# Optimization experiments

Hardware: AMD Instinct MI355X
Metric: run time of the kernel (lower is better)

## Reference

```python
import jax, jax.numpy as jnp
import numpy as np

D_MODEL = 1024
NUM_HEADS = 16
D_K = D_MODEL // NUM_HEADS


def setup_inputs() -> dict:
    key = jax.random.key(0)
    ks = jax.random.split(key, 9)
    s = 1.0 / np.sqrt(D_MODEL)
    x = jax.random.normal(ks[0], (4, 2048, D_MODEL), dtype=jnp.float32)
    Wq = jax.random.uniform(ks[1], (D_MODEL, D_MODEL), jnp.float32, -s, s)
    bq = jax.random.uniform(ks[2], (D_MODEL,), jnp.float32, -s, s)
    Wk = jax.random.uniform(ks[3], (D_MODEL, D_MODEL), jnp.float32, -s, s)
    bk = jax.random.uniform(ks[4], (D_MODEL,), jnp.float32, -s, s)
    Wv = jax.random.uniform(ks[5], (D_MODEL, D_MODEL), jnp.float32, -s, s)
    bv = jax.random.uniform(ks[6], (D_MODEL,), jnp.float32, -s, s)
    Wo = jax.random.uniform(ks[7], (D_MODEL, D_MODEL), jnp.float32, -s, s)
    bo = jax.random.uniform(ks[8], (D_MODEL,), jnp.float32, -s, s)
    return {"x": x, "Wq": Wq, "bq": bq, "Wk": Wk, "bk": bk,
            "Wv": Wv, "bv": bv, "Wo": Wo, "bo": bo}


def reference(x, Wq, bq, Wk, bk, Wv, bv, Wo, bo):
    B, S, _ = x.shape
    # Linear projections (torch Linear: x @ W.T + b)
    q = x @ Wq.T + bq
    k = x @ Wk.T + bk
    v = x @ Wv.T + bv
    # [B, H, S, d_k]
    q = q.reshape(B, S, NUM_HEADS, D_K).transpose(0, 2, 1, 3)
    k = k.reshape(B, S, NUM_HEADS, D_K).transpose(0, 2, 1, 3)
    v = v.reshape(B, S, NUM_HEADS, D_K).transpose(0, 2, 1, 3)
    score = jnp.einsum('bhqd,bhkd->bhqk', q, k) / jnp.sqrt(jnp.float32(D_K))
    causal = jnp.tril(jnp.ones((S, S), dtype=bool))  # True = keep
    score = jnp.where(causal[None, None], score, -jnp.inf)
    attn = jax.nn.softmax(score, axis=-1)
    out = jnp.einsum('bhqk,bhkd->bhqd', attn, v)
    out = out.transpose(0, 2, 1, 3).reshape(B, S, D_MODEL)
    return out @ Wo.T + bo
```

## Files before the change

### kernel.cpp

```cpp
#include <hip/hip_runtime.h>
#include <hip/hip_bf16.h>
#include <stdint.h>

#define D_MODEL 1024
#define SEQ     2048
#define BATCH   4
#define NHEAD   16
#define DKH     64
#define MTOT    (BATCH * SEQ)

typedef __bf16 bf16x8 __attribute__((ext_vector_type(8)));
typedef __bf16 bf16x4 __attribute__((ext_vector_type(4)));
typedef float  floatx4 __attribute__((ext_vector_type(4)));
typedef short  s16x4  __attribute__((ext_vector_type(4)));

#define GLOAD_LDS16(gp, lp)                                            \
    __builtin_amdgcn_global_load_lds(                                  \
        (const __attribute__((address_space(1))) unsigned int*)(gp),   \
        (__attribute__((address_space(3))) unsigned int*)(lp), 16, 0, 0)

#define MFMA16(a, b, c) __builtin_amdgcn_mfma_f32_16x16x32_bf16(a, b, c, 0, 0, 0)

#if __has_builtin(__builtin_amdgcn_exp2f)
#define EXP2(x) __builtin_amdgcn_exp2f(x)
#else
#define EXP2(x) exp2f(x)
#endif

static __device__ __forceinline__ floatx4 pv_mfma(s16x4 a, s16x4 b, floatx4 c)
{
#if __has_builtin(__builtin_amdgcn_mfma_f32_16x16x16bf16_1k)
    return __builtin_amdgcn_mfma_f32_16x16x16bf16_1k(a, b, c, 0, 0, 0);
#else
    asm("v_mfma_f32_16x16x16_bf16 %0, %1, %2, %0" : "+v"(c) : "v"(a), "v"(b));
    return c;
#endif
}

__global__ __launch_bounds__(256)
void cvt_x_kernel(const float* __restrict__ src, __bf16* __restrict__ dst)
{
    const int i = (blockIdx.x * 256 + threadIdx.x) * 4;
    floatx4 v = *(const floatx4*)(src + i);
    bf16x4 o;
    o[0] = (__bf16)v[0]; o[1] = (__bf16)v[1]; o[2] = (__bf16)v[2]; o[3] = (__bf16)v[3];
    *(bf16x4*)(dst + i) = o;
}

__global__ __launch_bounds__(256)
void cvt_w3_kernel(const float* __restrict__ Wq, const float* __restrict__ Wk,
                   const float* __restrict__ Wv, __bf16* __restrict__ Wcat)
{
    const int z = blockIdx.y;
    const float* src = (z == 0) ? Wq : ((z == 1) ? Wk : Wv);
    const int i = (blockIdx.x * 256 + threadIdx.x) * 4;
    floatx4 v = *(const floatx4*)(src + i);
    bf16x4 o;
    o[0] = (__bf16)v[0]; o[1] = (__bf16)v[1]; o[2] = (__bf16)v[2]; o[3] = (__bf16)v[3];
    *(bf16x4*)(Wcat + (size_t)z * (D_MODEL * D_MODEL) + i) = o;
}

__global__ __launch_bounds__(256)
void qkv_gemm_kernel(const __bf16* __restrict__ xb, const __bf16* __restrict__ Wcat,
                     const float* __restrict__ bq, const float* __restrict__ bk,
                     const float* __restrict__ bv,
                     __bf16* __restrict__ Q, __bf16* __restrict__ K,
                     __bf16* __restrict__ Vt)
{
    __shared__ __align__(16) char smem_raw[128 * 136 * 2];
    __bf16* As = (__bf16*)smem_raw;
    __bf16* Bs = (__bf16*)(smem_raw + 16384);
    __bf16* Cs = (__bf16*)smem_raw;

    const int t    = threadIdx.x;
    const int w    = t >> 6, l = t & 63, quad = l >> 4, r16 = l & 15;
    const int wm   = w & 1, wn = w >> 1;
    const int m0   = blockIdx.y * 128;
    const int n0   = blockIdx.x * 128;
    const int z    = n0 >> 10;
    const float* bias = (z == 0) ? bq : ((z == 1) ? bk : bv);
    __bf16* outQK     = (z == 0) ? Q  : K;
    const float scale = (z == 0) ? 0.18033688011112042f : 1.0f;

    floatx4 acc[4][4];
#pragma unroll
    for (int i = 0; i < 4; ++i)
#pragma unroll
        for (int j = 0; j < 4; ++j) acc[i][j] = (floatx4){0.f, 0.f, 0.f, 0.f};

    unsigned int* lAs = (unsigned int*)As;
    unsigned int* lBs = (unsigned int*)Bs;

    const int r0 = t >> 3;
    const int s0 = ((t & 7) ^ (r0 & 7)) * 8;
    const __bf16* Agp[4];
    const __bf16* Bgp[4];
#pragma unroll
    for (int i = 0; i < 4; ++i) {
        const int row = r0 + i * 32;
        const int sch8 = ((t & 7) ^ (row & 7)) * 8;
        Agp[i] = xb   + (size_t)(m0 + row) * 1024 + sch8;
        Bgp[i] = Wcat + (size_t)(n0 + row) * 1024 + sch8;
    }
    (void)s0;

    const int fsw0 = ((0 * 4 + quad) ^ (r16 & 7)) * 8;
    const int fsw1 = ((1 * 4 + quad) ^ (r16 & 7)) * 8;

    for (int k0 = 0; k0 < 1024; k0 += 64) {
        __syncthreads();
#pragma unroll
        for (int i = 0; i < 4; ++i) {
            const int c = t + 256 * i;
            GLOAD_LDS16(Agp[i] + k0, lAs + c * 4);
            GLOAD_LDS16(Bgp[i] + k0, lBs + c * 4);
        }
        __syncthreads();

#pragma unroll
        for (int kk = 0; kk < 2; ++kk) {
            const int fsw = (kk == 0) ? fsw0 : fsw1;
            bf16x8 af[4], bfm[4];
#pragma unroll
            for (int i = 0; i < 4; ++i)
                af[i] = *(const bf16x8*)&As[(wm * 64 + i * 16 + r16) * 64 + fsw];
#pragma unroll
            for (int j = 0; j < 4; ++j)
                bfm[j] = *(const bf16x8*)&Bs[(wn * 64 + j * 16 + r16) * 64 + fsw];
#pragma unroll
            for (int i = 0; i < 4; ++i)
#pragma unroll
                for (int j = 0; j < 4; ++j)
                    acc[i][j] = MFMA16(af[i], bfm[j], acc[i][j]);
        }
    }

    __syncthreads();

    if (z == 2) {
#pragma unroll
        for (int i = 0; i < 4; ++i) {
            const int mb = wm * 64 + i * 16 + quad * 4;
#pragma unroll
            for (int j = 0; j < 4; ++j) {
                const int nl = wn * 64 + j * 16 + r16;
                const float bb = bias[(n0 + nl) & 1023];
                bf16x4 p4;
#pragma unroll
                for (int r = 0; r < 4; ++r) p4[r] = (__bf16)(acc[i][j][r] + bb);
                *(bf16x4*)&Cs[nl * 136 + mb] = p4;
            }
        }
    } else {
#pragma unroll
        for (int i = 0; i < 4; ++i) {
            const int mb = wm * 64 + i * 16 + quad * 4;
#pragma unroll
            for (int j = 0; j < 4; ++j) {
                const int nl = wn * 64 + j * 16 + r16;
                const float bb = bias[(n0 + nl) & 1023];
#pragma unroll
                for (int r = 0; r < 4; ++r)
                    Cs[(mb + r) * 136 + nl] =
                        (__bf16)((acc[i][j][r] + bb) * scale);
            }
        }
    }
    __syncthreads();

    const int b  = m0 >> 11;
    if (z == 2) {
#pragma unroll
        for (int k = 0; k < 8; ++k) {
            const int nl = (t >> 4) + k * 16;
            const int ml = (t & 15) * 8;
            bf16x8 row = *(const bf16x8*)&Cs[nl * 136 + ml];
            const int f = (n0 + nl) & 1023, h = f >> 6, d = f & 63;
            const int s = (m0 & 2047) + ml;
            *(bf16x8*)&Vt[((size_t)((b * 16 + h) * 64 + d) << 11) + s] = row;
        }
    } else {
#pragma unroll
        for (int k = 0; k < 8; ++k) {
            const int ml = (t >> 4) + k * 16;
            const int nl = (t & 15) * 8;
            bf16x8 row = *(const bf16x8*)&Cs[ml * 136 + nl];
            const int f = (n0 + nl) & 1023, h = f >> 6, d = f & 63;
            const int s = (m0 & 2047) + ml;
            *(bf16x8*)&outQK[((size_t)(b * 16 + h) << 17) + ((size_t)s << 6) + d]
                = row;
        }
    }
}

__global__ __launch_bounds__(256)
void out_gemm_kernel(const __bf16* __restrict__ A, const __bf16* __restrict__ Wob,
                     const float* __restrict__ bo, float* __restrict__ out)
{
    __shared__ __align__(16) __bf16 As[128 * 64];
    __shared__ __align__(16) __bf16 Bs[128 * 64];

    const int t    = threadIdx.x;
    const int w    = t >> 6, l = t & 63, quad = l >> 4, r16 = l & 15;
    const int wm   = w & 1, wn = w >> 1;
    const int m0   = blockIdx.y * 128;
    const int n0   = blockIdx.x * 128;

    floatx4 acc[4][4];
#pragma unroll
    for (int i = 0; i < 4; ++i)
#pragma unroll
        for (int j = 0; j < 4; ++j) acc[i][j] = (floatx4){0.f, 0.f, 0.f, 0.f};

    unsigned int* lAs = (unsigned int*)As;
    unsigned int* lBs = (unsigned int*)Bs;

    const int r0 = t >> 3;
    const __bf16* Agp[4];
    const __bf16* Bgp[4];
#pragma unroll
    for (int i = 0; i < 4; ++i) {
        const int row = r0 + i * 32;
        const int sch8 = ((t & 7) ^ (row & 7)) * 8;
        Agp[i] = A   + (size_t)(m0 + row) * 1024 + sch8;
        Bgp[i] = Wob + (size_t)(n0 + row) * 1024 + sch8;
    }
    const int fsw0 = ((0 * 4 + quad) ^ (r16 & 7)) * 8;
    const int fsw1 = ((1 * 4 + quad) ^ (r16 & 7)) * 8;

    for (int k0 = 0; k0 < 1024; k0 += 64) {
        __syncthreads();
#pragma unroll
        for (int i = 0; i < 4; ++i) {
            const int c = t + 256 * i;
            GLOAD_LDS16(Agp[i] + k0, lAs + c * 4);
            GLOAD_LDS16(Bgp[i] + k0, lBs + c * 4);
        }
        __syncthreads();

#pragma unroll
        for (int kk = 0; kk < 2; ++kk) {
            const int fsw = (kk == 0) ? fsw0 : fsw1;
            bf16x8 af[4], bfm[4];
#pragma unroll
            for (int i = 0; i < 4; ++i)
                af[i] = *(const bf16x8*)&As[(wm * 64 + i * 16 + r16) * 64 + fsw];
#pragma unroll
            for (int j = 0; j < 4; ++j)
                bfm[j] = *(const bf16x8*)&Bs[(wn * 64 + j * 16 + r16) * 64 + fsw];
#pragma unroll
            for (int i = 0; i < 4; ++i)
#pragma unroll
                for (int j = 0; j < 4; ++j)
                    acc[i][j] = MFMA16(af[i], bfm[j], acc[i][j]);
        }
    }

#pragma unroll
    for (int i = 0; i < 4; ++i) {
        const int mg = m0 + wm * 64 + i * 16 + quad * 4;
#pragma unroll
        for (int j = 0; j < 4; ++j) {
            const int ng = n0 + wn * 64 + j * 16 + r16;
            const float bb = bo[ng];
#pragma unroll
            for (int r = 0; r < 4; ++r)
                out[(size_t)(mg + r) * 1024 + ng] = acc[i][j][r] + bb;
        }
    }
}

__global__ __launch_bounds__(256, 4)
void attn_kernel(const __bf16* __restrict__ Qg, const __bf16* __restrict__ Kg,
                 const __bf16* __restrict__ Vtg, __bf16* __restrict__ O)
{
    __shared__ __align__(16) __bf16 Ks[2][64 * 72];
    __shared__ __align__(16) __bf16 Vs[2][64 * 72];

    const int t    = threadIdx.x;
    const int w    = t >> 6, l = t & 63, quad = l >> 4, r16 = l & 15;
    const int bh   = blockIdx.x;
    const int y    = blockIdx.y;
    const int p    = y >> 1, half = y & 1;
    const int qa   = 15 - p, qb = p;
    const size_t base = (size_t)bh * SEQ * DKH;
    const int d0   = 2 * qa + half;
    const int d1   = 2 * qb + half;
    const int nkt  = d0 + 1;
    const int row0 = qa * 128 + half * 64 + w * 16;
    const int row1 = qb * 128 + half * 64 + w * 16;

    const s16x4 ones16 = {(short)0x3F80, (short)0x3F80,
                          (short)0x3F80, (short)0x3F80};

    bf16x8 qf00, qf01, qf10, qf11;
    qf00 = *(const bf16x8*)&Qg[base + (size_t)(row0 + r16) * 64 + quad * 8];
    qf01 = *(const bf16x8*)&Qg[base + (size_t)(row0 + r16) * 64 + 32 + quad * 8];
    qf10 = *(const bf16x8*)&Qg[base + (size_t)(row1 + r16) * 64 + quad * 8];
    qf11 = *(const bf16x8*)&Qg[base + (size_t)(row1 + r16) * 64 + 32 + quad * 8];

    floatx4 o[2][4];
#pragma unroll
    for (int mi = 0; mi < 2; ++mi)
#pragma unroll
        for (int j = 0; j < 4; ++j) o[mi][j] = (floatx4){0.f, 0.f, 0.f, 0.f};
    floatx4 osum[2];
    osum[0] = (floatx4){0.f, 0.f, 0.f, 0.f};
    osum[1] = (floatx4){0.f, 0.f, 0.f, 0.f};

    const int srow = t >> 3;
    const int sg   = (t & 7) * 8;

    bf16x8 kc0, kc1, vc0, vc1;
    kc0 = *(const bf16x8*)&Kg[base + (size_t)srow * 64 + sg];
    kc1 = *(const bf16x8*)&Kg[base + (size_t)(32 + srow) * 64 + sg];
    vc0 = *(const bf16x8*)&Vtg[base + (size_t)srow * 2048 + sg];
    vc1 = *(const bf16x8*)&Vtg[base + (size_t)(32 + srow) * 2048 + sg];

    for (int kt = 0; kt < nkt; ++kt) {
        __bf16* ks = Ks[kt & 1];
        __bf16* vs = Vs[kt & 1];
        *(bf16x8*)&ks[srow * 72 + sg] = kc0;
        *(bf16x8*)&ks[(32 + srow) * 72 + sg] = kc1;
        *(bf16x8*)&vs[srow * 72 + sg] = vc0;
        *(bf16x8*)&vs[(32 + srow) * 72 + sg] = vc1;
        if (kt + 1 < nkt) {
            const int kr = (kt + 1) * 64;
            kc0 = *(const bf16x8*)&Kg[base + (size_t)(kr + srow) * 64 + sg];
            kc1 = *(const bf16x8*)&Kg[base + (size_t)(kr + 32 + srow) * 64 + sg];
            vc0 = *(const bf16x8*)&Vtg[base + (size_t)srow * 2048 + kr + sg];
            vc1 = *(const bf16x8*)&Vtg[base + (size_t)(32 + srow) * 2048 + kr + sg];
        }
        __syncthreads();

        const bool a1 = (kt <= d1);
        __builtin_amdgcn_s_setprio(1);
        bf16x8 kf0, kf1;
#pragma unroll
        for (int j = 0; j < 4; ++j) {
            kf0 = *(const bf16x8*)&ks[(j * 16 + r16) * 72 + quad * 8];
            kf1 = *(const bf16x8*)&ks[(j * 16 + r16) * 72 + 32 + quad * 8];
            floatx4 z0 = (floatx4){0.f, 0.f, 0.f, 0.f};
            floatx4 z1 = (floatx4){0.f, 0.f, 0.f, 0.f};
            z0 = MFMA16(kf0, qf00, z0);
            z0 = MFMA16(kf1, qf01, z0);
            if (a1) {
                z1 = MFMA16(kf0, qf10, z1);
                z1 = MFMA16(kf1, qf11, z1);
            }
            const int kg = kt * 64 + j * 16 + quad * 4;
            bf16x4 pb0, pb1;
            if (kt < d0) {
#pragma unroll
                for (int r = 0; r < 4; ++r)
                    pb0[r] = (__bf16)EXP2(z0[r]);
            } else {
                const int qg0 = row0 + r16;
#pragma unroll
                for (int r = 0; r < 4; ++r) {
                    float pp = 0.f;
                    if (kg + r <= qg0) pp = EXP2(z0[r]);
                    pb0[r] = (__bf16)pp;
                }
            }
            s16x4 pa0 = __builtin_bit_cast(s16x4, pb0);
            s16x4 pa1;
            if (a1) {
                if (kt < d1) {
#pragma unroll
                    for (int r = 0; r < 4; ++r)
                        pb1[r] = (__bf16)EXP2(z1[r]);
                } else {
                    const int qg1 = row1 + r16;
#pragma unroll
                    for (int r = 0; r < 4; ++r) {
                        float pp = 0.f;
                        if (kg + r <= qg1) pp = EXP2(z1[r]);
                        pb1[r] = (__bf16)pp;
                    }
                }
                pa1 = __builtin_bit_cast(s16x4, pb1);
            }
            osum[0] = pv_mfma(pa0, ones16, osum[0]);
            if (a1) osum[1] = pv_mfma(pa1, ones16, osum[1]);
#pragma unroll
            for (int jd = 0; jd < 4; ++jd) {
                const s16x4 vv =
                    *(const s16x4*)&vs[(jd * 16 + r16) * 72 + j * 16 + quad * 4];
                o[0][jd] = pv_mfma(pa0, vv, o[0][jd]);
                if (a1) o[1][jd] = pv_mfma(pa1, vv, o[1][jd]);
            }
        }
        __builtin_amdgcn_s_setprio(0);
    }

    const int b = bh >> 4, h = bh & 15;
#pragma unroll
    for (int mi = 0; mi < 2; ++mi) {
        const int rowb = (mi == 0) ? row0 : row1;
#pragma unroll
        for (int r = 0; r < 4; ++r) {
            const int qrow = rowb + quad * 4 + r;
            const float inv = 1.f / osum[mi][r];
#pragma unroll
            for (int jd = 0; jd < 4; ++jd) {
                const int d = jd * 16 + r16;
                O[((size_t)(b * SEQ + qrow) * D_MODEL) + h * 64 + d] =
                    (__bf16)(o[mi][jd][r] * inv);
            }
        }
    }
}

extern "C" void kernel_launch(void* const* d_in, const int* in_sizes, int n_in,
                              void* d_out, int out_size, void* d_ws, size_t ws_size,
                              hipStream_t stream)
{
    (void)in_sizes; (void)n_in; (void)out_size; (void)ws_size;
    const float* x  = (const float*)d_in[0];
    const float* Wq = (const float*)d_in[1];
    const float* bq = (const float*)d_in[2];
    const float* Wk = (const float*)d_in[3];
    const float* bk = (const float*)d_in[4];
    const float* Wv = (const float*)d_in[5];
    const float* bv = (const float*)d_in[6];
    const float* Wo = (const float*)d_in[7];
    const float* bo = (const float*)d_in[8];
    float* out = (float*)d_out;

    const size_t n_elem = (size_t)MTOT * D_MODEL;
    const int    w_n    = D_MODEL * D_MODEL;
    __bf16* Qb  = (__bf16*)d_out;
    __bf16* xb  = Qb + n_elem;
    __bf16* Kb   = (__bf16*)d_ws;
    __bf16* Vtb  = Kb + n_elem;
    __bf16* Ab   = Vtb + n_elem;
    __bf16* Wcat = Ab;
    __bf16* Wob  = Kb;

    cvt_x_kernel<<<MTOT * D_MODEL / 1024, 256, 0, stream>>>(x, xb);
    cvt_w3_kernel<<<dim3(w_n / 1024, 3), 256, 0, stream>>>(Wq, Wk, Wv, Wcat);
    qkv_gemm_kernel<<<dim3(24, 64), 256, 0, stream>>>(xb, Wcat, bq, bk, bv,
                                                      Qb, Kb, Vtb);
    attn_kernel<<<dim3(64, 16), 256, 0, stream>>>(Qb, Kb, Vtb, Ab);
    cvt_x_kernel<<<w_n / 1024, 256, 0, stream>>>(Wo, Wob);
    out_gemm_kernel<<<dim3(8, 64), 256, 0, stream>>>(Ab, Wob, bo, out);
}
```

Measured before the change: 245.3 us.

## Shrink QKV GEMM LDS footprint for occupancy and merge input conversion launches

The QKV GEMM K-tile drops from 64 to 32, cutting shared memory to about 17 KB. The epilogue now writes C in two half-tile passes through the same small buffer, and the launch bounds request 6 blocks per CU to raise occupancy. The x and Wq/Wk/Wv fp32-to-bf16 conversions are merged into one launch to remove a kernel launch. In exchange, the GEMM runs twice as many barrier-separated K iterations with less work per iteration, and the epilogue adds extra syncs.

```diff
diff --git a/kernel.cpp b/kernel.cpp
--- a/kernel.cpp
+++ b/kernel.cpp
@@ -38,6 +38,30 @@
 }
 
 __global__ __launch_bounds__(256)
+void cvt_pre_kernel(const float* __restrict__ x, const float* __restrict__ Wq,
+                    const float* __restrict__ Wk, const float* __restrict__ Wv,
+                    __bf16* __restrict__ xb, __bf16* __restrict__ Wcat)
+{
+    int bid = blockIdx.x;
+    const float* src;
+    __bf16* dst;
+    if (bid < 8192) {
+        src = x;  dst = xb;
+    } else {
+        bid -= 8192;
+        const int z = bid >> 10;
+        bid &= 1023;
+        src = (z == 0) ? Wq : ((z == 1) ? Wk : Wv);
+        dst = Wcat + (size_t)z * (D_MODEL * D_MODEL);
+    }
+    const int i = (bid * 256 + threadIdx.x) * 4;
+    floatx4 v = *(const floatx4*)(src + i);
+    bf16x4 o;
+    o[0] = (__bf16)v[0]; o[1] = (__bf16)v[1]; o[2] = (__bf16)v[2]; o[3] = (__bf16)v[3];
+    *(bf16x4*)(dst + i) = o;
+}
+
+__global__ __launch_bounds__(256)
 void cvt_x_kernel(const float* __restrict__ src, __bf16* __restrict__ dst)
 {
     const int i = (blockIdx.x * 256 + threadIdx.x) * 4;
@@ -47,30 +71,17 @@
     *(bf16x4*)(dst + i) = o;
 }
 
-__global__ __launch_bounds__(256)
-void cvt_w3_kernel(const float* __restrict__ Wq, const float* __restrict__ Wk,
-                   const float* __restrict__ Wv, __bf16* __restrict__ Wcat)
-{
-    const int z = blockIdx.y;
-    const float* src = (z == 0) ? Wq : ((z == 1) ? Wk : Wv);
-    const int i = (blockIdx.x * 256 + threadIdx.x) * 4;
-    floatx4 v = *(const floatx4*)(src + i);
-    bf16x4 o;
-    o[0] = (__bf16)v[0]; o[1] = (__bf16)v[1]; o[2] = (__bf16)v[2]; o[3] = (__bf16)v[3];
-    *(bf16x4*)(Wcat + (size_t)z * (D_MODEL * D_MODEL) + i) = o;
-}
-
-__global__ __launch_bounds__(256)
+__global__ __launch_bounds__(256, 6)
 void qkv_gemm_kernel(const __bf16* __restrict__ xb, const __bf16* __restrict__ Wcat,
                      const float* __restrict__ bq, const float* __restrict__ bk,
                      const float* __restrict__ bv,
                      __bf16* __restrict__ Q, __bf16* __restrict__ K,
                      __bf16* __restrict__ Vt)
 {
-    __shared__ __align__(16) char smem_raw[128 * 136 * 2];
-    __bf16* As = (__bf16*)smem_raw;
-    __bf16* Bs = (__bf16*)(smem_raw + 16384);
-    __bf16* Cs = (__bf16*)smem_raw;
+    __shared__ __align__(16) char smem_raw[17408];
+    __bf16* As  = (__bf16*)smem_raw;
+    __bf16* Bs  = (__bf16*)(smem_raw + 8192);
+    __bf16* Csh = (__bf16*)smem_raw;
 
     const int t    = threadIdx.x;
     const int w    = t >> 6, l = t & 63, quad = l >> 4, r16 = l & 15;
@@ -88,107 +99,104 @@
 #pragma unroll
         for (int j = 0; j < 4; ++j) acc[i][j] = (floatx4){0.f, 0.f, 0.f, 0.f};
 
+    const int c0 = t, c1 = t + 256;
+    const int row0 = c0 >> 2, s0 = ((c0 & 3) ^ (row0 & 3)) * 8;
+    const int row1 = c1 >> 2, s1 = ((c1 & 3) ^ (row1 & 3)) * 8;
+    const __bf16* Ag0 = xb   + (size_t)(m0 + row0) * 1024 + s0;
+    const __bf16* Ag1 = xb   + (size_t)(m0 + row1) * 1024 + s1;
+    const __bf16* Bg0 = Wcat + (size_t)(n0 + row0) * 1024 + s0;
+    const __bf16* Bg1 = Wcat + (size_t)(n0 + row1) * 1024 + s1;
     unsigned int* lAs = (unsigned int*)As;
     unsigned int* lBs = (unsigned int*)Bs;
 
-    const int r0 = t >> 3;
-    const int s0 = ((t & 7) ^ (r0 & 7)) * 8;
-    const __bf16* Agp[4];
-    const __bf16* Bgp[4];
-#pragma unroll
-    for (int i = 0; i < 4; ++i) {
-        const int row = r0 + i * 32;
-        const int sch8 = ((t & 7) ^ (row & 7)) * 8;
-        Agp[i] = xb   + (size_t)(m0 + row) * 1024 + sch8;
-        Bgp[i] = Wcat + (size_t)(n0 + row) * 1024 + sch8;
-    }
-    (void)s0;
-
-    const int fsw0 = ((0 * 4 + quad) ^ (r16 & 7)) * 8;
-    const int fsw1 = ((1 * 4 + quad) ^ (r16 & 7)) * 8;
-
-    for (int k0 = 0; k0 < 1024; k0 += 64) {
+    const int fsw = (quad ^ (r16 & 3)) * 8;
+
+    for (int k0 = 0; k0 < 1024; k0 += 32) {
         __syncthreads();
-#pragma unroll
-        for (int i = 0; i < 4; ++i) {
-            const int c = t + 256 * i;
-            GLOAD_LDS16(Agp[i] + k0, lAs + c * 4);
-            GLOAD_LDS16(Bgp[i] + k0, lBs + c * 4);
-        }
+        GLOAD_LDS16(Ag0 + k0, lAs + c0 * 4);
+        GLOAD_LDS16(Ag1 + k0, lAs + c1 * 4);
+        GLOAD_LDS16(Bg0 + k0, lBs + c0 * 4);
+        GLOAD_LDS16(Bg1 + k0, lBs + c1 * 4);
         __syncthreads();
 
-#pragma unroll
-        for (int kk = 0; kk < 2; ++kk) {
-            const int fsw = (kk == 0) ? fsw0 : fsw1;
-            bf16x8 af[4], bfm[4];
-#pragma unroll
-            for (int i = 0; i < 4; ++i)
-                af[i] = *(const bf16x8*)&As[(wm * 64 + i * 16 + r16) * 64 + fsw];
+        bf16x8 af[4], bfm[4];
+#pragma unroll
+        for (int i = 0; i < 4; ++i)
+            af[i] = *(const bf16x8*)&As[(wm * 64 + i * 16 + r16) * 32 + fsw];
+#pragma unroll
+        for (int j = 0; j < 4; ++j)
+            bfm[j] = *(const bf16x8*)&Bs[(wn * 64 + j * 16 + r16) * 32 + fsw];
+#pragma unroll
+        for (int i = 0; i < 4; ++i)
 #pragma unroll
             for (int j = 0; j < 4; ++j)
-                bfm[j] = *(const bf16x8*)&Bs[(wn * 64 + j * 16 + r16) * 64 + fsw];
-#pragma unroll
-            for (int i = 0; i < 4; ++i)
-#pragma unroll
-                for (int j = 0; j < 4; ++j)
-                    acc[i][j] = MFMA16(af[i], bfm[j], acc[i][j]);
-        }
-    }
-
-    __syncthreads();
-
+                acc[i][j] = MFMA16(af[i], bfm[j], acc[i][j]);
+    }
+
+    const int b = m0 >> 11;
     if (z == 2) {
 #pragma unroll
-        for (int i = 0; i < 4; ++i) {
-            const int mb = wm * 64 + i * 16 + quad * 4;
-#pragma unroll
-            for (int j = 0; j < 4; ++j) {
-                const int nl = wn * 64 + j * 16 + r16;
-                const float bb = bias[(n0 + nl) & 1023];
-                bf16x4 p4;
-#pragma unroll
-                for (int r = 0; r < 4; ++r) p4[r] = (__bf16)(acc[i][j][r] + bb);
-                *(bf16x4*)&Cs[nl * 136 + mb] = p4;
+        for (int pass = 0; pass < 2; ++pass) {
+            __syncthreads();
+            if (wn == pass) {
+#pragma unroll
+                for (int i = 0; i < 4; ++i) {
+                    const int mb = wm * 64 + i * 16 + quad * 4;
+#pragma unroll
+                    for (int j = 0; j < 4; ++j) {
+                        const int nl = j * 16 + r16;
+                        const float bb = bias[(n0 + pass * 64 + nl) & 1023];
+                        bf16x4 p4;
+#pragma unroll
+                        for (int r = 0; r < 4; ++r)
+                            p4[r] = (__bf16)(acc[i][j][r] + bb);
+                        *(bf16x4*)&Csh[nl * 136 + mb] = p4;
+                    }
+                }
+            }
+            __syncthreads();
+#pragma unroll
+            for (int k = 0; k < 4; ++k) {
+                const int nll = (t >> 4) + k * 16;
+                const int ml  = (t & 15) * 8;
+                bf16x8 rowv = *(const bf16x8*)&Csh[nll * 136 + ml];
+                const int f = (n0 + pass * 64 + nll) & 1023;
+                const int h = f >> 6, d = f & 63;
+                const int s = (m0 & 2047) + ml;
+                *(bf16x8*)&Vt[((size_t)((b * 16 + h) * 64 + d) << 11) + s] = rowv;
             }
         }
     } else {
 #pragma unroll
-        for (int i = 0; i < 4; ++i) {
-            const int mb = wm * 64 + i * 16 + quad * 4;
-#pragma unroll
-            for (int j = 0; j < 4; ++j) {
-                const int nl = wn * 64 + j * 16 + r16;
-                const float bb = bias[(n0 + nl) & 1023];
-#pragma unroll
-                for (int r = 0; r < 4; ++r)
-                    Cs[(mb + r) * 136 + nl] =
-                        (__bf16)((acc[i][j][r] + bb) * scale);
-            }
-        }
-    }
-    __syncthreads();
-
-    const int b  = m0 >> 11;
-    if (z == 2) {
-#pragma unroll
-        for (int k = 0; k < 8; ++k) {
-            const int nl = (t >> 4) + k * 16;
-            const int ml = (t & 15) * 8;
-            bf16x8 row = *(const bf16x8*)&Cs[nl * 136 + ml];
-            const int f = (n0 + nl) & 1023, h = f >> 6, d = f & 63;
-            const int s = (m0 & 2047) + ml;
-            *(bf16x8*)&Vt[((size_t)((b * 16 + h) * 64 + d) << 11) + s] = row;
-        }
-    } else {
-#pragma unroll
-        for (int k = 0; k < 8; ++k) {
-            const int ml = (t >> 4) + k * 16;
-            const int nl = (t & 15) * 8;
-            bf16x8 row = *(const bf16x8*)&Cs[ml * 136 + nl];
-            const int f = (n0 + nl) & 1023, h = f >> 6, d = f & 63;
-            const int s = (m0 & 2047) + ml;
-            *(bf16x8*)&outQK[((size_t)(b * 16 + h) << 17) + ((size_t)s << 6) + d]
-                = row;
+        for (int pass = 0; pass < 2; ++pass) {
+            __syncthreads();
+            if (wm == pass) {
+#pragma unroll
+                for (int i = 0; i < 4; ++i) {
+                    const int mbl = i * 16 + quad * 4;
+#pragma unroll
+                    for (int j = 0; j < 4; ++j) {
+                        const int nl = wn * 64 + j * 16 + r16;
+                        const float bb = bias[(n0 + nl) & 1023];
+#pragma unroll
+                        for (int r = 0; r < 4; ++r)
+                            Csh[(mbl + r) * 136 + nl] =
+                                (__bf16)((acc[i][j][r] + bb) * scale);
+                    }
+                }
+            }
+            __syncthreads();
+#pragma unroll
+            for (int k = 0; k < 4; ++k) {
+                const int mll = (t >> 4) + k * 16;
+                const int nl  = (t & 15) * 8;
+                bf16x8 rowv = *(const bf16x8*)&Csh[mll * 136 + nl];
+                const int f = (n0 + nl) & 1023;
+                const int h = f >> 6, d = f & 63;
+                const int s = (m0 & 2047) + pass * 64 + mll;
+                *(bf16x8*)&outQK[((size_t)(b * 16 + h) << 17) + ((size_t)s << 6) + d]
+                    = rowv;
+            }
         }
     }
 }
@@ -438,8 +446,7 @@
     __bf16* Wcat = Ab;
     __bf16* Wob  = Kb;
 
-    cvt_x_kernel<<<MTOT * D_MODEL / 1024, 256, 0, stream>>>(x, xb);
-    cvt_w3_kernel<<<dim3(w_n / 1024, 3), 256, 0, stream>>>(Wq, Wk, Wv, Wcat);
+    cvt_pre_kernel<<<8192 + 3072, 256, 0, stream>>>(x, Wq, Wk, Wv, xb, Wcat);
     qkv_gemm_kernel<<<dim3(24, 64), 256, 0, stream>>>(xb, Wcat, bq, bk, bv,
                                                       Qb, Kb, Vtb);
     attn_kernel<<<dim3(64, 16), 256, 0, stream>>>(Qb, Kb, Vtb, Ab);
```

Result: slower. 576.5 us (+135.0%).
